# Optimization experiments

Measured on AMD Instinct MI355X. Metric: run time of the kernel, lower is better.

The kernel has to match this reference:

```python
import jax, jax.numpy as jnp
import numpy as np
import math

S, H, NH, HD = 2048, 1280, 16, 80
WIN = 64
NW = S // WIN
I = 3420
OUT = 3584
L = 8
FULL_IDX = (3, 7)
MERGE = 4  # spatial_merge_size**2
EPS = 1e-6


def setup_inputs() -> dict:
    key = jax.random.key(0)
    ks = jax.random.split(key, 16)
    w = lambda k, s: jax.random.normal(k, s, jnp.float32) * 0.02
    # rotary tables: half-dim freqs duplicated, as in Qwen2.5-VL vision rotary
    inv_freq = 1.0 / (10000.0 ** (np.arange(0, HD // 2, dtype=np.float32) / (HD // 2)))
    freqs = np.outer(np.arange(S, dtype=np.float32), inv_freq)  # [S, HD/2]
    emb = np.concatenate([freqs, freqs], axis=-1)               # [S, HD]
    return {
        "hidden_states": jax.random.normal(ks[0], (S, H), jnp.float32),
        "full_attn_masks": jnp.ones((1, 1, S, S), jnp.float32),
        "window_attn_masks": jnp.ones((NW, 1, WIN, WIN), jnp.float32),
        "cos": jnp.asarray(np.cos(emb)),
        "sin": jnp.asarray(np.sin(emb)),
        "qkv_w": w(ks[1], (L, 3 * H, H)),
        "qkv_b": w(ks[2], (L, 3 * H)),
        "proj_w": w(ks[3], (L, H, H)),
        "proj_b": w(ks[4], (L, H)),
        "norm1_w": jnp.ones((L, H), jnp.float32),
        "norm2_w": jnp.ones((L, H), jnp.float32),
        "gate_w": w(ks[5], (L, I, H)),
        "gate_b": w(ks[6], (L, I)),
        "up_w": w(ks[7], (L, I, H)),
        "up_b": w(ks[8], (L, I)),
        "down_w": w(ks[9], (L, H, I)),
        "down_b": w(ks[10], (L, H)),
        "ln_q_w": jnp.ones((H,), jnp.float32),
        "m0_w": w(ks[11], (H * MERGE, H * MERGE)),
        "m0_b": w(ks[12], (H * MERGE,)),
        "m2_w": w(ks[13], (OUT, H * MERGE)),
        "m2_b": w(ks[14], (OUT,)),
    }


def rmsnorm(x, w):
    v = jnp.mean(jnp.square(x.astype(jnp.float32)), axis=-1, keepdims=True)
    return (x * jax.lax.rsqrt(v + EPS)) * w


def rotate_half(x):
    x1, x2 = jnp.split(x, 2, axis=-1)
    return jnp.concatenate([-x2, x1], axis=-1)


def apply_rope(q, k, cos, sin):
    return q * cos + rotate_half(q) * sin, k * cos + rotate_half(k) * sin


def attn_full(x, mask, cos, sin, qkv_w, qkv_b, proj_w, proj_b):
    # x: [S, H]; mask: [1, 1, S, S] (additive)
    qkv = (x @ qkv_w.T + qkv_b).reshape(S, 3, NH, HD)
    q, k, v = [t[:, i].transpose(1, 0, 2) for i, t in [(0, qkv), (1, qkv), (2, qkv)]]  # [NH, S, HD]
    q, k = apply_rope(q, k, cos, sin)  # cos/sin [S, HD] broadcast over heads
    aw = jnp.einsum('hsd,htd->hst', q, k) / math.sqrt(HD) + mask[0]
    aw = jax.nn.softmax(aw.astype(jnp.float32), axis=-1)
    o = jnp.einsum('hst,htd->hsd', aw, v).transpose(1, 0, 2).reshape(S, NH * HD)
    return o @ proj_w.T + proj_b


def attn_window(x, mask, cos, sin, qkv_w, qkv_b, proj_w, proj_b):
    xw = x.reshape(NW, WIN, H)
    qkv = (xw @ qkv_w.T + qkv_b).reshape(NW, WIN, 3, NH, HD).transpose(2, 0, 3, 1, 4)
    q, k, v = qkv[0], qkv[1], qkv[2]
    cw = cos.reshape(NW, 1, WIN, HD)
    sw = sin.reshape(NW, 1, WIN, HD)
    q, k = apply_rope(q, k, cw, sw)
    aw = jnp.einsum('whsd,whtd->whst', q, k) / math.sqrt(HD) + mask
    aw = jax.nn.softmax(aw.astype(jnp.float32), axis=-1)
    o = jnp.einsum('whst,whtd->whsd', aw, v).transpose(0, 2, 1, 3).reshape(S, NH * HD)
    return o @ proj_w.T + proj_b


def reference(hidden_states, full_attn_masks, window_attn_masks, cos, sin,
              qkv_w, qkv_b, proj_w, proj_b, norm1_w, norm2_w,
              gate_w, gate_b, up_w, up_b, down_w, down_b,
              ln_q_w, m0_w, m0_b, m2_w, m2_b):
    NEG = jnp.finfo(jnp.float32).min
    fm = (1.0 - full_attn_masks) * NEG
    wm = (1.0 - window_attn_masks) * NEG
    x = hidden_states
    for i in range(L):
        h = rmsnorm(x, norm1_w[i])
        if i in FULL_IDX:
            a = attn_full(h, fm, cos, sin, qkv_w[i], qkv_b[i], proj_w[i], proj_b[i])
        else:
            a = attn_window(h, wm, cos, sin, qkv_w[i], qkv_b[i], proj_w[i], proj_b[i])
        x = x + a
        h = rmsnorm(x, norm2_w[i])
        mlp = (jax.nn.silu(h @ gate_w[i].T + gate_b[i]) * (h @ up_w[i].T + up_b[i])) @ down_w[i].T + down_b[i]
        x = x + mlp
    # patch merger: RMSNorm -> merge 4 tokens -> Linear-GELU-Linear
    h = rmsnorm(x, ln_q_w).reshape(-1, H * MERGE)  # [S/4, 5120]
    h = jax.nn.gelu(h @ m0_w.T + m0_b, approximate=False)
    return h @ m2_w.T + m2_b  # [S/4, OUT]
```

## Files before the change

kernel.cpp:

```cpp
#include <hip/hip_runtime.h>
#include <hip/hip_bf16.h>
#include <math.h>

#define S_LEN 2048
#define HID   1280
#define NHEADS 16
#define HDIM  80
#define HDP   96
#define VROWS 96
#define LAYERS 8
#define IDIM  3420
#define IDIMP 3456
#define MERGED 5120
#define OUTD  3584
#define LWE   19824640LL

typedef __attribute__((ext_vector_type(8))) short short8;
typedef __attribute__((ext_vector_type(4))) float f32x4;
typedef __attribute__((ext_vector_type(16))) float f32x16;
typedef unsigned int u32;
typedef __attribute__((ext_vector_type(4))) u32 u32x4;
typedef __attribute__((address_space(1))) const u32* gptr_t;
typedef __attribute__((address_space(3))) u32* lptr_t;

__device__ inline unsigned short f2b(float f){
  __hip_bfloat16 b = __float2bfloat16(f);
  return __builtin_bit_cast(unsigned short, b);
}
__device__ inline float b2f(unsigned short u){
  return __bfloat162float(__builtin_bit_cast(__hip_bfloat16, u));
}
__device__ inline unsigned pk2(float lo, float hi){
  return (unsigned)f2b(lo) | ((unsigned)f2b(hi) << 16);
}

#define NSEG 42
struct ConvSegs {
  int bpre[NSEG + 1];
  long long srcoff[NSEG];
  long long dstoff[NSEG];
  int srcbase[NSEG];
  int N[NSEG], K[NSEG], Kp[NSEG];
  int rstride[NSEG], roffs[NSEG];
};

__global__ __launch_bounds__(256) void convert_all_kernel(
    ConvSegs cs, int bstart,
    const float* __restrict__ b0, const float* __restrict__ b1,
    const float* __restrict__ b2, const float* __restrict__ b3,
    const float* __restrict__ b4, const float* __restrict__ b5,
    const float* __restrict__ b6,
    unsigned short* __restrict__ dst)
{
  const int b = blockIdx.x + bstart;
  int seg = 0;
  while (seg < NSEG - 1 && cs.bpre[seg + 1] <= b) ++seg;
  const int Kp = cs.Kp[seg], K = cs.K[seg], N = cs.N[seg];
  const int kg = Kp >> 3;
  size_t g = (size_t)(b - cs.bpre[seg]) * 256 + threadIdx.x;
  int k8 = (int)(g % kg);
  int n  = (int)(g / kg);
  int k0 = k8 * 8;
  const float* base;
  switch (cs.srcbase[seg]){
    case 0: base = b0; break; case 1: base = b1; break;
    case 2: base = b2; break; case 3: base = b3; break;
    case 4: base = b4; break; case 5: base = b5; break;
    default: base = b6; break;
  }
  const float* src = base + cs.srcoff[seg];
  u32 out0, out1, out2, out3;
  if (n < N && k0 + 8 <= K){
    const float* s = src + (size_t)n * K + k0;
    f32x4 f0 = __builtin_nontemporal_load((const f32x4*)s);
    f32x4 f1 = __builtin_nontemporal_load((const f32x4*)(s + 4));
    out0 = pk2(f0[0], f0[1]); out1 = pk2(f0[2], f0[3]);
    out2 = pk2(f1[0], f1[1]); out3 = pk2(f1[2], f1[3]);
  } else {
    u32 tmp[4];
    #pragma unroll
    for (int j = 0; j < 4; ++j){
      int ka = k0 + 2 * j;
      float lv = (n < N && ka     < K) ? src[(size_t)n * K + ka]     : 0.f;
      float hv = (n < N && ka + 1 < K) ? src[(size_t)n * K + ka + 1] : 0.f;
      tmp[j] = pk2(lv, hv);
    }
    out0 = tmp[0]; out1 = tmp[1]; out2 = tmp[2]; out3 = tmp[3];
  }
  size_t de = (size_t)cs.dstoff[seg] +
              ((size_t)n * cs.rstride[seg] + cs.roffs[seg]) * Kp + k0;
  u32x4 ov = {out0, out1, out2, out3};
  __builtin_nontemporal_store(ov, (u32x4*)(dst + de));
}

__global__ __launch_bounds__(256) void concat_bias_kernel(
    const float* __restrict__ g, const float* __restrict__ u, float* __restrict__ o)
{
  int L = blockIdx.y;
  int n = blockIdx.x * 256 + threadIdx.x;
  if (n >= 2 * IDIMP) return;
  int c = n >> 1, which = n & 1;
  float v = 0.f;
  if (c < IDIM) v = which ? u[(size_t)L * IDIM + c] : g[(size_t)L * IDIM + c];
  o[(size_t)L * 2 * IDIMP + n] = v;
}

__global__ __launch_bounds__(256) void rmsnorm_kernel(
    const float* __restrict__ x, const float* __restrict__ w,
    unsigned short* __restrict__ out, int H)
{
  int s = blockIdx.x;
  const float* row = x + (size_t)s * H;
  float ss = 0.f;
  for (int c = threadIdx.x; c < H; c += 256){ float v = row[c]; ss += v * v; }
  #pragma unroll
  for (int off = 32; off >= 1; off >>= 1) ss += __shfl_xor(ss, off, 64);
  __shared__ float red[4];
  if ((threadIdx.x & 63) == 0) red[threadIdx.x >> 6] = ss;
  __syncthreads();
  ss = red[0] + red[1] + red[2] + red[3];
  float rs = rsqrtf(ss / H + 1e-6f);
  unsigned short* orow = out + (size_t)s * H;
  for (int c = threadIdx.x; c < H; c += 256) orow[c] = f2b(row[c] * rs * w[c]);
}

template<int EPI, int BM, int BN>
__global__ __launch_bounds__(256) void gemm_kernel(
    const unsigned short* __restrict__ A, int lda,
    const unsigned short* __restrict__ B, int ldb,
    const float* __restrict__ bias, int Nact,
    void* __restrict__ Cv, int ldc,
    const float* __restrict__ res,
    int K)
{
  constexpr int MI = BM / 32;
  constexpr int NI = BN / 32;
  __shared__ __align__(16) unsigned short As[2][BM * 32];
  __shared__ __align__(16) unsigned short Bs[2][BN * 32];
  const int tid  = threadIdx.x;
  const int lane = tid & 63;
  const int wave = tid >> 6;
  const int wm = wave >> 1, wn = wave & 1;
  const int gx = gridDim.x, gy = gridDim.y;
  const int total = gx * gy;
  const int orig = blockIdx.y * gx + blockIdx.x;
  const int q8 = total >> 3, r8 = total & 7;
  const int xcd = orig & 7, loc = orig >> 3;
  const int wg = (xcd < r8 ? xcd * (q8 + 1) : r8 * (q8 + 1) + (xcd - r8) * q8) + loc;
  const int m0 = (wg % gy) * BM, n0 = (wg / gy) * BN;
  const int l16 = lane & 15, lh = lane >> 4;
  const int lrow = lane >> 2;
  const int lcol = lane & 3;
  f32x4 acc[MI][NI] = {};

  auto stage = [&](int bufi, int k0){
    #pragma unroll
    for (int j = 0; j < BM / 64; ++j){
      int chunk = wave * (BM / 64) + j;
      int row  = chunk * 16 + lrow;
      int slot = lcol ^ ((row >> 1) & 3);
      const unsigned short* srcA = A + (size_t)(m0 + row) * lda + k0 + slot * 8;
      __builtin_amdgcn_global_load_lds((gptr_t)srcA, (lptr_t)&As[bufi][chunk * 512], 16, 0, 0);
    }
    #pragma unroll
    for (int j = 0; j < BN / 64; ++j){
      int chunk = wave * (BN / 64) + j;
      int row  = chunk * 16 + lrow;
      int slot = lcol ^ ((row >> 1) & 3);
      const unsigned short* srcB = B + (size_t)(n0 + row) * ldb + k0 + slot * 8;
      __builtin_amdgcn_global_load_lds((gptr_t)srcB, (lptr_t)&Bs[bufi][chunk * 512], 16, 0, 0);
    }
  };

  const int nt = K >> 5;
  stage(0, 0);
  __syncthreads();
  int buf = 0;
  for (int t = 0; t < nt; ++t){
    if (t + 1 < nt) stage(buf ^ 1, (t + 1) << 5);
    short8 af[MI], bfr[NI];
    #pragma unroll
    for (int mi = 0; mi < MI; ++mi){
      int r = wm * (BM / 2) + mi * 16 + l16;
      int sl = lh ^ ((r >> 1) & 3);
      af[mi] = *(const short8*)&As[buf][r * 32 + sl * 8];
    }
    #pragma unroll
    for (int ni = 0; ni < NI; ++ni){
      int r = wn * (BN / 2) + ni * 16 + l16;
      int sl = lh ^ ((r >> 1) & 3);
      bfr[ni] = *(const short8*)&Bs[buf][r * 32 + sl * 8];
    }
    #pragma unroll
    for (int mi = 0; mi < MI; ++mi)
      #pragma unroll
      for (int ni = 0; ni < NI; ++ni)
        acc[mi][ni] = __builtin_amdgcn_mfma_f32_16x16x32_bf16(af[mi], bfr[ni], acc[mi][ni], 0, 0, 0);
    __syncthreads();
    buf ^= 1;
  }

  #pragma unroll
  for (int mi = 0; mi < MI; ++mi){
    int row = m0 + wm * (BM / 2) + mi * 16 + lh * 4;
    #pragma unroll
    for (int ni = 0; ni < NI; ++ni){
      int gn = n0 + wn * (BN / 2) + ni * 16 + l16;
      float bv = (gn < Nact) ? bias[gn] : 0.f;
      #pragma unroll
      for (int r2 = 0; r2 < 4; ++r2){
        float v = acc[mi][ni][r2] + bv;
        if (EPI == 4){
          float partner = __shfl_xor(v, 1);
          if (!(l16 & 1)){
            float r = v / (1.f + __expf(-v)) * partner;
            ((unsigned short*)Cv)[(size_t)(row + r2) * ldc + (gn >> 1)] = f2b(r);
          }
        } else {
          size_t offc = (size_t)(row + r2) * ldc + gn;
          if (EPI == 0)      ((float*)Cv)[offc] = v;
          else if (EPI == 1) ((float*)Cv)[offc] = res[offc] + v;
          else if (EPI == 2) ((unsigned short*)Cv)[offc] = f2b(0.5f * v * (1.0f + erff(v * 0.70710678118f)));
          else               ((unsigned short*)Cv)[offc] = f2b(v);
        }
      }
    }
  }
}

__global__ __launch_bounds__(256) void rope_split_kernel(
    const unsigned short* __restrict__ qkv, const float* __restrict__ cosT,
    const float* __restrict__ sinT,
    unsigned short* __restrict__ qo, unsigned short* __restrict__ ko,
    unsigned short* __restrict__ vt)
{
  __shared__ unsigned short vtile[80][128];
  int id = blockIdx.y * 16 + blockIdx.x;
  int logical = ((id & 7) << 5) + (id >> 3);
  const int h = logical & 15;
  const int s0 = (logical >> 4) * 128;
  const int t = threadIdx.x;
  const int sr = t >> 1, half = t & 1;
  const int s = s0 + sr;
  const unsigned short* row = qkv + (size_t)s * 3840 + h * 80;
  const float* crow = cosT + (size_t)s * 80;
  const float* srow = sinT + (size_t)s * 80;
  const float sgn = half ? 1.f : -1.f;
  #pragma unroll
  for (int g = 0; g < 5; ++g){
    int d  = half * 40 + g * 8;
    int dp = 40 - half * 40 + g * 8;
    short8 q8  = *(const short8*)(row + d);
    short8 k8  = *(const short8*)(row + 1280 + d);
    short8 qp8 = *(const short8*)(row + dp);
    short8 kp8 = *(const short8*)(row + 1280 + dp);
    short8 v8  = *(const short8*)(row + 2560 + d);
    f32x4 c0  = *(const f32x4*)(crow + d);
    f32x4 c1  = *(const f32x4*)(crow + d + 4);
    f32x4 sn0 = *(const f32x4*)(srow + d);
    f32x4 sn1 = *(const f32x4*)(srow + d + 4);
    float cc[8] = {c0[0], c0[1], c0[2], c0[3], c1[0], c1[1], c1[2], c1[3]};
    float ss[8] = {sn0[0], sn0[1], sn0[2], sn0[3], sn1[0], sn1[1], sn1[2], sn1[3]};
    short8 qo8, ko8;
    #pragma unroll
    for (int j = 0; j < 8; ++j){
      float qv = b2f((unsigned short)q8[j]);
      float kv = b2f((unsigned short)k8[j]);
      float qr = sgn * b2f((unsigned short)qp8[j]);
      float kr = sgn * b2f((unsigned short)kp8[j]);
      qo8[j] = (short)f2b(qv * cc[j] + qr * ss[j]);
      ko8[j] = (short)f2b(kv * cc[j] + kr * ss[j]);
      vtile[d + j][sr] = (unsigned short)v8[j];
    }
    size_t qkoff = ((size_t)h * S_LEN + s) * HDP + d;
    *(short8*)(qo + qkoff) = qo8;
    *(short8*)(ko + qkoff) = ko8;
  }
  {
    short8 z = {};
    size_t poff = ((size_t)h * S_LEN + s) * HDP + 80 + half * 8;
    *(short8*)(qo + poff) = z;
    *(short8*)(ko + poff) = z;
  }
  __syncthreads();
  #pragma unroll
  for (int it = 0; it < 5; ++it){
    int j = t + it * 256;
    int d = j >> 4, ch = j & 15;
    u32x4 v = *(const u32x4*)&vtile[d][ch * 8];
    *(u32x4*)(vt + ((size_t)h * VROWS + d) * S_LEN + s0 + ch * 8) = v;
  }
}

template<int PART>
__global__ __launch_bounds__(256) void flash_kernel(
    const unsigned short* __restrict__ q, const unsigned short* __restrict__ k,
    const unsigned short* __restrict__ vt, unsigned short* __restrict__ out)
{
  const int lane = threadIdx.x & 63;
  const int w = threadIdx.x >> 6;
  const int l31 = lane & 31, lh1 = lane >> 5;
  int h, qr;
  if (PART){
    int id = blockIdx.y * gridDim.x + blockIdx.x;
    int logical = ((id & 7) << 7) + (id >> 3);
    h = logical >> 6; qr = (logical & 63) * 32;
  } else {
    int id = blockIdx.y * gridDim.x + blockIdx.x;
    int logical = ((id & 7) << 5) + (id >> 3);
    h = logical >> 4; qr = (logical & 15) * 128 + w * 32;
  }
  const unsigned short* qh = q + (size_t)h * S_LEN * HDP;
  const unsigned short* kh = k + (size_t)h * S_LEN * HDP;
  const unsigned short* vh = vt + (size_t)h * VROWS * S_LEN;

  short8 qa[5];
  #pragma unroll
  for (int kc = 0; kc < 5; ++kc)
    qa[kc] = *(const short8*)(qh + (size_t)(qr + l31) * HDP + kc * 16 + lh1 * 8);

  float m_ = -1e30f, l_ = 0.f;
  f32x16 o0 = {}, o1 = {}, o2 = {};
  const int kvb = PART ? w * 512 : (qr & ~63);
  const int kve = PART ? w * 512 + 512 : (qr & ~63) + 64;
  const float scale = 0.11180339887498949f;

  for (int kvt = kvb; kvt < kve; kvt += 32){
    f32x16 sc = {};
    __builtin_amdgcn_s_setprio(1);
    #pragma unroll
    for (int kc = 0; kc < 5; ++kc){
      short8 kf = *(const short8*)(kh + (size_t)(kvt + l31) * HDP + kc * 16 + lh1 * 8);
      sc = __builtin_amdgcn_mfma_f32_32x32x16_bf16(kf, qa[kc], sc, 0, 0, 0);
    }
    __builtin_amdgcn_s_setprio(0);
    float t = sc[0];
    #pragma unroll
    for (int i = 1; i < 16; ++i) t = fmaxf(t, sc[i]);
    t = fmaxf(t, __shfl_xor(t, 32)) * scale;
    if (!__all(t <= m_ + 8.f)){
      float mnew = fmaxf(m_, t);
      float corr = __expf(m_ - mnew);
      l_ *= corr;
      #pragma unroll
      for (int i = 0; i < 16; ++i){ o0[i] *= corr; o1[i] *= corr; o2[i] *= corr; }
      m_ = mnew;
    }
    float p[16];
    float rs = 0.f;
    #pragma unroll
    for (int i = 0; i < 16; ++i){ p[i] = __expf(sc[i] * scale - m_); rs += p[i]; }
    rs += __shfl_xor(rs, 32);
    l_ += rs;
    unsigned wd0[4], wd1[4];
    #pragma unroll
    for (int j = 0; j < 2; ++j){
      unsigned Aj = pk2(p[2 * j],     p[2 * j + 1]);
      unsigned Bj = pk2(p[4 + 2 * j], p[4 + 2 * j + 1]);
      unsigned t0 = __shfl_xor(Aj, 32);
      unsigned t1 = __shfl_xor(Bj, 32);
      wd0[j]     = lh1 ? t1 : Aj;
      wd0[2 + j] = lh1 ? Bj : t0;
      Aj = pk2(p[8 + 2 * j],  p[8 + 2 * j + 1]);
      Bj = pk2(p[12 + 2 * j], p[12 + 2 * j + 1]);
      t0 = __shfl_xor(Aj, 32);
      t1 = __shfl_xor(Bj, 32);
      wd1[j]     = lh1 ? t1 : Aj;
      wd1[2 + j] = lh1 ? Bj : t0;
    }
    __builtin_amdgcn_s_setprio(1);
    #pragma unroll
    for (int kc2 = 0; kc2 < 2; ++kc2){
      u32x4 uw = kc2 ? u32x4{wd1[0], wd1[1], wd1[2], wd1[3]}
                     : u32x4{wd0[0], wd0[1], wd0[2], wd0[3]};
      short8 pb = __builtin_bit_cast(short8, uw);
      const unsigned short* vb = vh + kvt + kc2 * 16 + lh1 * 8;
      o0 = __builtin_amdgcn_mfma_f32_32x32x16_bf16(
          *(const short8*)(vb + (size_t)(l31)      * S_LEN), pb, o0, 0, 0, 0);
      o1 = __builtin_amdgcn_mfma_f32_32x32x16_bf16(
          *(const short8*)(vb + (size_t)(32 + l31) * S_LEN), pb, o1, 0, 0, 0);
      o2 = __builtin_amdgcn_mfma_f32_32x32x16_bf16(
          *(const short8*)(vb + (size_t)(64 + l31) * S_LEN), pb, o2, 0, 0, 0);
    }
    __builtin_amdgcn_s_setprio(0);
  }

  if (PART){
    __shared__ float of[80][33];
    __shared__ float mlsh[4][32][2];
    __shared__ float Lsh[32];
    __shared__ unsigned short ot2[32][88];
    if (lane < 32){ mlsh[w][l31][0] = m_; mlsh[w][l31][1] = l_; }
    __syncthreads();
    float M = fmaxf(fmaxf(mlsh[0][l31][0], mlsh[1][l31][0]),
                    fmaxf(mlsh[2][l31][0], mlsh[3][l31][0]));
    float L = 0.f;
    #pragma unroll
    for (int c = 0; c < 4; ++c) L += __expf(mlsh[c][l31][0] - M) * mlsh[c][l31][1];
    float wgt = __expf(m_ - M);
    if (w == 0 && lane < 32) Lsh[l31] = L;
    #pragma unroll
    for (int rnd = 0; rnd < 4; ++rnd){
      if (w == rnd){
        #pragma unroll
        for (int i = 0; i < 16; ++i){
          int dl = (i & 3) + 8 * (i >> 2) + 4 * lh1;
          if (rnd == 0){
            of[dl][l31]      = wgt * o0[i];
            of[32 + dl][l31] = wgt * o1[i];
            if (dl < 16) of[64 + dl][l31] = wgt * o2[i];
          } else {
            of[dl][l31]      += wgt * o0[i];
            of[32 + dl][l31] += wgt * o1[i];
            if (dl < 16) of[64 + dl][l31] += wgt * o2[i];
          }
        }
      }
      __syncthreads();
    }
    const int tq = threadIdx.x & 31, ds0 = (threadIdx.x >> 5) * 10;
    float Lq = Lsh[tq];
    #pragma unroll
    for (int j = 0; j < 10; ++j)
      ot2[tq][ds0 + j] = f2b(of[ds0 + j][tq] / Lq);
    __syncthreads();
    if (threadIdx.x < 64){
      int qq = threadIdx.x >> 1, half = threadIdx.x & 1;
      #pragma unroll
      for (int j2 = 0; j2 < 20; ++j2){
        unsigned v = *(const unsigned*)&ot2[qq][half * 40 + j2 * 2];
        *(unsigned*)&out[(size_t)(qr + qq) * HID + h * HDIM + half * 40 + j2 * 2] = v;
      }
    }
  } else {
    __shared__ unsigned short ot[4][32][88];
    float inv = 1.f / l_;
    #pragma unroll
    for (int r = 0; r < 16; ++r){
      int dl = (r & 3) + 8 * (r >> 2) + 4 * lh1;
      ot[w][l31][dl]      = f2b(o0[r] * inv);
      ot[w][l31][32 + dl] = f2b(o1[r] * inv);
      if (dl < 16) ot[w][l31][64 + dl] = f2b(o2[r] * inv);
    }
    int qq = lane >> 1, half = lane & 1;
    #pragma unroll
    for (int j = 0; j < 20; ++j){
      unsigned v = *(const unsigned*)&ot[w][qq][half * 40 + j * 2];
      *(unsigned*)&out[(size_t)(qr + qq) * HID + h * HDIM + half * 40 + j * 2] = v;
    }
  }
}

extern "C" void kernel_launch(void* const* d_in, const int* in_sizes, int n_in,
                              void* d_out, int out_size, void* d_ws, size_t ws_size,
                              hipStream_t stream)
{
  const float* hidden = (const float*)d_in[0];
  const float* cosT   = (const float*)d_in[3];
  const float* sinT   = (const float*)d_in[4];
  const float* qkv_w  = (const float*)d_in[5];
  const float* qkv_b  = (const float*)d_in[6];
  const float* proj_w = (const float*)d_in[7];
  const float* proj_b = (const float*)d_in[8];
  const float* norm1_w= (const float*)d_in[9];
  const float* norm2_w= (const float*)d_in[10];
  const float* gate_w = (const float*)d_in[11];
  const float* gate_b = (const float*)d_in[12];
  const float* up_w   = (const float*)d_in[13];
  const float* up_b   = (const float*)d_in[14];
  const float* down_w = (const float*)d_in[15];
  const float* down_b = (const float*)d_in[16];
  const float* ln_q_w = (const float*)d_in[17];
  const float* m0_w   = (const float*)d_in[18];
  const float* m0_b   = (const float*)d_in[19];
  const float* m2_w   = (const float*)d_in[20];
  const float* m2_b   = (const float*)d_in[21];

  char* ws = (char*)d_ws;
  size_t off = 0;
  auto carve = [&](size_t bytes)->char*{
    char* p = ws + off; off += (bytes + 255) & ~(size_t)255; return p;
  };
  float*          x    = (float*)         carve((size_t)S_LEN * HID * 4);
  unsigned short* hbuf = (unsigned short*)carve((size_t)S_LEN * HID * 2);
  unsigned short* qkvb = (unsigned short*)carve((size_t)S_LEN * 3840 * 2);
  unsigned short* qp   = (unsigned short*)carve((size_t)NHEADS * S_LEN * HDP * 2);
  unsigned short* kp   = (unsigned short*)carve((size_t)NHEADS * S_LEN * HDP * 2);
  unsigned short* vtb  = (unsigned short*)carve((size_t)NHEADS * VROWS * S_LEN * 2);
  unsigned short* ao   = (unsigned short*)carve((size_t)S_LEN * HID * 2);
  unsigned short* mlp  = (unsigned short*)carve((size_t)S_LEN * IDIMP * 2);
  unsigned short* mg   = (unsigned short*)carve((size_t)512 * MERGED * 2);
  float*          cbias= (float*)         carve((size_t)LAYERS * 2 * IDIMP * 4);
  unsigned short* wbf  = (unsigned short*)carve((size_t)203161600 * 2);
  (void)ws_size; (void)in_sizes; (void)n_in; (void)out_size;

  ConvSegs cs;
  int totalblocks = 0;
  {
    int si = 0;
    auto add = [&](int base, long long soff, long long doff, int N, int K,
                   int Np, int Kp, int rstride, int roffs){
      cs.bpre[si] = totalblocks;
      cs.srcbase[si] = base; cs.srcoff[si] = soff; cs.dstoff[si] = doff;
      cs.N[si] = N; cs.K[si] = K; cs.Kp[si] = Kp;
      cs.rstride[si] = rstride; cs.roffs[si] = roffs;
      long long groups = (long long)Np * (Kp >> 3);
      totalblocks += (int)((groups + 255) / 256);
      ++si;
    };
    for (long long i = 0; i < LAYERS; ++i){
      add(0, i * 3840LL * HID,        i * LWE + 0,        3840, HID, 3840, HID, 1, 0);
      add(1, i * (long long)HID * HID, i * LWE + 4915200,  HID, HID, HID, HID, 1, 0);
      add(2, i * (long long)IDIM * HID, i * LWE + 6553600,  IDIM, HID, IDIMP, HID, 2, 0);
      add(3, i * (long long)IDIM * HID, i * LWE + 6553600,  IDIM, HID, IDIMP, HID, 2, 1);
      add(4, i * (long long)HID * IDIM, i * LWE + 15400960, HID, IDIM, HID, IDIMP, 1, 0);
    }
    add(5, 0, 8 * LWE,            MERGED, MERGED, MERGED, MERGED, 1, 0);
    add(6, 0, 8 * LWE + 26214400, OUTD,   MERGED, OUTD,   MERGED, 1, 0);
    cs.bpre[NSEG] = totalblocks;
  }

  {
    int chunk = (totalblocks + 3) / 4;
    for (int c = 0; c < 4; ++c){
      int bs = c * chunk;
      int nb = (bs + chunk <= totalblocks) ? chunk : (totalblocks - bs);
      if (nb > 0)
        convert_all_kernel<<<nb, 256, 0, stream>>>(
            cs, bs, qkv_w, proj_w, gate_w, up_w, down_w, m0_w, m2_w, wbf);
    }
  }
  concat_bias_kernel<<<dim3(27, LAYERS), 256, 0, stream>>>(gate_b, up_b, cbias);
  hipMemcpyAsync(x, hidden, (size_t)S_LEN * HID * 4, hipMemcpyDeviceToDevice, stream);

  for (int i = 0; i < LAYERS; ++i){
    unsigned short* wl = wbf + (size_t)i * LWE;
    unsigned short* wqkv = wl;
    unsigned short* wproj= wl + 4915200;
    unsigned short* wgu  = wl + 6553600;
    unsigned short* wdown= wl + 15400960;

    rmsnorm_kernel<<<S_LEN, 256, 0, stream>>>(x, norm1_w + (size_t)i * HID, hbuf, HID);
    gemm_kernel<3,128,128><<<dim3(30, 16), 256, 0, stream>>>(
        hbuf, HID, wqkv, HID, qkv_b + (size_t)i * 3840, 3840,
        qkvb, 3840, nullptr, HID);
    rope_split_kernel<<<dim3(NHEADS, 16), 256, 0, stream>>>(qkvb, cosT, sinT, qp, kp, vtb);
    if (i == 3 || i == 7){
      flash_kernel<1><<<dim3(64, 16), 256, 0, stream>>>(qp, kp, vtb, ao);
    } else {
      flash_kernel<0><<<dim3(16, 16), 256, 0, stream>>>(qp, kp, vtb, ao);
    }
    gemm_kernel<1,64,64><<<dim3(20, 32), 256, 0, stream>>>(
        ao, HID, wproj, HID, proj_b + (size_t)i * HID, HID,
        x, HID, x, HID);
    rmsnorm_kernel<<<S_LEN, 256, 0, stream>>>(x, norm2_w + (size_t)i * HID, hbuf, HID);
    gemm_kernel<4,128,128><<<dim3(54, 16), 256, 0, stream>>>(
        hbuf, HID, wgu, HID, cbias + (size_t)i * 2 * IDIMP, 2 * IDIMP,
        mlp, IDIMP, nullptr, HID);
    gemm_kernel<1,64,64><<<dim3(20, 32), 256, 0, stream>>>(
        mlp, IDIMP, wdown, IDIMP, down_b + (size_t)i * HID, HID,
        x, HID, x, IDIMP);
  }
  unsigned short* wm0 = wbf + 8 * LWE;
  unsigned short* wm2 = wm0 + (size_t)MERGED * MERGED;
  rmsnorm_kernel<<<S_LEN, 256, 0, stream>>>(x, ln_q_w, hbuf, HID);
  gemm_kernel<2,64,64><<<dim3(80, 8), 256, 0, stream>>>(
      hbuf, MERGED, wm0, MERGED, m0_b, MERGED, mg, MERGED, nullptr, MERGED);
  gemm_kernel<0,64,64><<<dim3(56, 8), 256, 0, stream>>>(
      mg, MERGED, wm2, MERGED, m2_b, OUTD, d_out, OUTD, nullptr, MERGED);
}
```

Baseline: 2.465 ms.

## Fuse RoPE and split into window attention kernel via shared memory

For the window-attention layers, a new kernel applies rotary embedding to q/k and transposes v straight into shared memory, then runs the 64-token window attention from LDS. This removes the separate rope_split launch and the global-memory round trip of padded q, k and transposed v for those layers. Full-attention layers keep the old path, now as a dedicated non-templated kernel. In exchange the fused kernel uses a large shared-memory footprint, which may lower occupancy.

```diff
diff --git a/kernel.cpp b/kernel.cpp
--- a/kernel.cpp
+++ b/kernel.cpp
@@ -292,54 +292,103 @@
   }
 }
 
-template<int PART>
-__global__ __launch_bounds__(256) void flash_kernel(
-    const unsigned short* __restrict__ q, const unsigned short* __restrict__ k,
-    const unsigned short* __restrict__ vt, unsigned short* __restrict__ out)
+#define QKPAD 104
+#define VPAD  136
+__global__ __launch_bounds__(256) void rope_window_kernel(
+    const unsigned short* __restrict__ qkv, const float* __restrict__ cosT,
+    const float* __restrict__ sinT, unsigned short* __restrict__ out)
 {
-  const int lane = threadIdx.x & 63;
-  const int w = threadIdx.x >> 6;
+  __shared__ __align__(16) unsigned short qs[128][QKPAD];
+  __shared__ __align__(16) unsigned short ks[128][QKPAD];
+  __shared__ __align__(16) unsigned short vtile[96][VPAD];
+  __shared__ unsigned short ot[4][32][88];
+  int id = blockIdx.y * 16 + blockIdx.x;
+  int logical = ((id & 7) << 5) + (id >> 3);
+  const int h = logical & 15;
+  const int s0 = (logical >> 4) * 128;
+  const int t = threadIdx.x;
+  {
+    const int sr = t >> 1, half = t & 1;
+    const int s = s0 + sr;
+    const unsigned short* row = qkv + (size_t)s * 3840 + h * 80;
+    const float* crow = cosT + (size_t)s * 80;
+    const float* srow = sinT + (size_t)s * 80;
+    const float sgn = half ? 1.f : -1.f;
+    #pragma unroll
+    for (int g = 0; g < 5; ++g){
+      int d  = half * 40 + g * 8;
+      int dp = 40 - half * 40 + g * 8;
+      short8 q8  = *(const short8*)(row + d);
+      short8 k8  = *(const short8*)(row + 1280 + d);
+      short8 qp8 = *(const short8*)(row + dp);
+      short8 kp8 = *(const short8*)(row + 1280 + dp);
+      short8 v8  = *(const short8*)(row + 2560 + d);
+      f32x4 c0  = *(const f32x4*)(crow + d);
+      f32x4 c1  = *(const f32x4*)(crow + d + 4);
+      f32x4 sn0 = *(const f32x4*)(srow + d);
+      f32x4 sn1 = *(const f32x4*)(srow + d + 4);
+      float cc[8] = {c0[0], c0[1], c0[2], c0[3], c1[0], c1[1], c1[2], c1[3]};
+      float ss[8] = {sn0[0], sn0[1], sn0[2], sn0[3], sn1[0], sn1[1], sn1[2], sn1[3]};
+      short8 qo8, ko8;
+      #pragma unroll
+      for (int j = 0; j < 8; ++j){
+        float qv = b2f((unsigned short)q8[j]);
+        float kv = b2f((unsigned short)k8[j]);
+        float qr = sgn * b2f((unsigned short)qp8[j]);
+        float kr = sgn * b2f((unsigned short)kp8[j]);
+        qo8[j] = (short)f2b(qv * cc[j] + qr * ss[j]);
+        ko8[j] = (short)f2b(kv * cc[j] + kr * ss[j]);
+        vtile[d + j][sr] = (unsigned short)v8[j];
+      }
+      *(short8*)&qs[sr][d] = qo8;
+      *(short8*)&ks[sr][d] = ko8;
+    }
+    short8 z = {};
+    *(short8*)&qs[sr][80 + half * 8] = z;
+    *(short8*)&ks[sr][80 + half * 8] = z;
+    #pragma unroll
+    for (int r9 = 0; r9 < 2; ++r9){
+      int task = t + r9 * 256;
+      if (task < 16 * 17){
+        int rr = task / 17, cc2 = (task % 17) * 8;
+        *(short8*)&vtile[80 + rr][cc2] = z;
+      }
+    }
+  }
+  __syncthreads();
+
+  const int lane = t & 63;
+  const int w = t >> 6;
   const int l31 = lane & 31, lh1 = lane >> 5;
-  int h, qr;
-  if (PART){
-    int id = blockIdx.y * gridDim.x + blockIdx.x;
-    int logical = ((id & 7) << 7) + (id >> 3);
-    h = logical >> 6; qr = (logical & 63) * 32;
-  } else {
-    int id = blockIdx.y * gridDim.x + blockIdx.x;
-    int logical = ((id & 7) << 5) + (id >> 3);
-    h = logical >> 4; qr = (logical & 15) * 128 + w * 32;
-  }
-  const unsigned short* qh = q + (size_t)h * S_LEN * HDP;
-  const unsigned short* kh = k + (size_t)h * S_LEN * HDP;
-  const unsigned short* vh = vt + (size_t)h * VROWS * S_LEN;
+  const int qrl = w * 32;
+  const int kv0 = (w >> 1) * 64;
 
   short8 qa[5];
   #pragma unroll
   for (int kc = 0; kc < 5; ++kc)
-    qa[kc] = *(const short8*)(qh + (size_t)(qr + l31) * HDP + kc * 16 + lh1 * 8);
+    qa[kc] = *(const short8*)&qs[qrl + l31][kc * 16 + lh1 * 8];
 
   float m_ = -1e30f, l_ = 0.f;
   f32x16 o0 = {}, o1 = {}, o2 = {};
-  const int kvb = PART ? w * 512 : (qr & ~63);
-  const int kve = PART ? w * 512 + 512 : (qr & ~63) + 64;
   const float scale = 0.11180339887498949f;
 
-  for (int kvt = kvb; kvt < kve; kvt += 32){
+  #pragma unroll
+  for (int step = 0; step < 2; ++step){
+    int kvl = kv0 + step * 32;
     f32x16 sc = {};
     __builtin_amdgcn_s_setprio(1);
     #pragma unroll
     for (int kc = 0; kc < 5; ++kc){
-      short8 kf = *(const short8*)(kh + (size_t)(kvt + l31) * HDP + kc * 16 + lh1 * 8);
+      short8 kf = *(const short8*)&ks[kvl + l31][kc * 16 + lh1 * 8];
       sc = __builtin_amdgcn_mfma_f32_32x32x16_bf16(kf, qa[kc], sc, 0, 0, 0);
     }
     __builtin_amdgcn_s_setprio(0);
-    float t = sc[0];
-    #pragma unroll
-    for (int i = 1; i < 16; ++i) t = fmaxf(t, sc[i]);
-    t = fmaxf(t, __shfl_xor(t, 32)) * scale;
-    if (!__all(t <= m_ + 8.f)){
-      float mnew = fmaxf(m_, t);
+    float tmax = sc[0];
+    #pragma unroll
+    for (int i = 1; i < 16; ++i) tmax = fmaxf(tmax, sc[i]);
+    tmax = fmaxf(tmax, __shfl_xor(tmax, 32)) * scale;
+    if (!__all(tmax <= m_ + 8.f)){
+      float mnew = fmaxf(m_, tmax);
       float corr = __expf(m_ - mnew);
       l_ *= corr;
       #pragma unroll
@@ -374,6 +423,106 @@
       u32x4 uw = kc2 ? u32x4{wd1[0], wd1[1], wd1[2], wd1[3]}
                      : u32x4{wd0[0], wd0[1], wd0[2], wd0[3]};
       short8 pb = __builtin_bit_cast(short8, uw);
+      int sv = kvl + kc2 * 16 + lh1 * 8;
+      o0 = __builtin_amdgcn_mfma_f32_32x32x16_bf16(
+          *(const short8*)&vtile[l31][sv],      pb, o0, 0, 0, 0);
+      o1 = __builtin_amdgcn_mfma_f32_32x32x16_bf16(
+          *(const short8*)&vtile[32 + l31][sv], pb, o1, 0, 0, 0);
+      o2 = __builtin_amdgcn_mfma_f32_32x32x16_bf16(
+          *(const short8*)&vtile[64 + l31][sv], pb, o2, 0, 0, 0);
+    }
+    __builtin_amdgcn_s_setprio(0);
+  }
+
+  float inv = 1.f / l_;
+  #pragma unroll
+  for (int r = 0; r < 16; ++r){
+    int dl = (r & 3) + 8 * (r >> 2) + 4 * lh1;
+    ot[w][l31][dl]      = f2b(o0[r] * inv);
+    ot[w][l31][32 + dl] = f2b(o1[r] * inv);
+    if (dl < 16) ot[w][l31][64 + dl] = f2b(o2[r] * inv);
+  }
+  int qq = lane >> 1, half2 = lane & 1;
+  #pragma unroll
+  for (int j = 0; j < 20; ++j){
+    unsigned v = *(const unsigned*)&ot[w][qq][half2 * 40 + j * 2];
+    *(unsigned*)&out[(size_t)(s0 + qrl + qq) * HID + h * HDIM + half2 * 40 + j * 2] = v;
+  }
+}
+
+__global__ __launch_bounds__(256) void flash_full_kernel(
+    const unsigned short* __restrict__ q, const unsigned short* __restrict__ k,
+    const unsigned short* __restrict__ vt, unsigned short* __restrict__ out)
+{
+  const int lane = threadIdx.x & 63;
+  const int w = threadIdx.x >> 6;
+  const int l31 = lane & 31, lh1 = lane >> 5;
+  int id = blockIdx.y * gridDim.x + blockIdx.x;
+  int logical = ((id & 7) << 7) + (id >> 3);
+  const int h = logical >> 6;
+  const int qr = (logical & 63) * 32;
+  const unsigned short* qh = q + (size_t)h * S_LEN * HDP;
+  const unsigned short* kh = k + (size_t)h * S_LEN * HDP;
+  const unsigned short* vh = vt + (size_t)h * VROWS * S_LEN;
+
+  short8 qa[5];
+  #pragma unroll
+  for (int kc = 0; kc < 5; ++kc)
+    qa[kc] = *(const short8*)(qh + (size_t)(qr + l31) * HDP + kc * 16 + lh1 * 8);
+
+  float m_ = -1e30f, l_ = 0.f;
+  f32x16 o0 = {}, o1 = {}, o2 = {};
+  const float scale = 0.11180339887498949f;
+
+  for (int kvt = w * 512; kvt < w * 512 + 512; kvt += 32){
+    f32x16 sc = {};
+    __builtin_amdgcn_s_setprio(1);
+    #pragma unroll
+    for (int kc = 0; kc < 5; ++kc){
+      short8 kf = *(const short8*)(kh + (size_t)(kvt + l31) * HDP + kc * 16 + lh1 * 8);
+      sc = __builtin_amdgcn_mfma_f32_32x32x16_bf16(kf, qa[kc], sc, 0, 0, 0);
+    }
+    __builtin_amdgcn_s_setprio(0);
+    float t = sc[0];
+    #pragma unroll
+    for (int i = 1; i < 16; ++i) t = fmaxf(t, sc[i]);
+    t = fmaxf(t, __shfl_xor(t, 32)) * scale;
+    if (!__all(t <= m_ + 8.f)){
+      float mnew = fmaxf(m_, t);
+      float corr = __expf(m_ - mnew);
+      l_ *= corr;
+      #pragma unroll
+      for (int i = 0; i < 16; ++i){ o0[i] *= corr; o1[i] *= corr; o2[i] *= corr; }
+      m_ = mnew;
+    }
+    float p[16];
+    float rs = 0.f;
+    #pragma unroll
+    for (int i = 0; i < 16; ++i){ p[i] = __expf(sc[i] * scale - m_); rs += p[i]; }
+    rs += __shfl_xor(rs, 32);
+    l_ += rs;
+    unsigned wd0[4], wd1[4];
+    #pragma unroll
+    for (int j = 0; j < 2; ++j){
+      unsigned Aj = pk2(p[2 * j],     p[2 * j + 1]);
+      unsigned Bj = pk2(p[4 + 2 * j], p[4 + 2 * j + 1]);
+      unsigned t0 = __shfl_xor(Aj, 32);
+      unsigned t1 = __shfl_xor(Bj, 32);
+      wd0[j]     = lh1 ? t1 : Aj;
+      wd0[2 + j] = lh1 ? Bj : t0;
+      Aj = pk2(p[8 + 2 * j],  p[8 + 2 * j + 1]);
+      Bj = pk2(p[12 + 2 * j], p[12 + 2 * j + 1]);
+      t0 = __shfl_xor(Aj, 32);
+      t1 = __shfl_xor(Bj, 32);
+      wd1[j]     = lh1 ? t1 : Aj;
+      wd1[2 + j] = lh1 ? Bj : t0;
+    }
+    __builtin_amdgcn_s_setprio(1);
+    #pragma unroll
+    for (int kc2 = 0; kc2 < 2; ++kc2){
+      u32x4 uw = kc2 ? u32x4{wd1[0], wd1[1], wd1[2], wd1[3]}
+                     : u32x4{wd0[0], wd0[1], wd0[2], wd0[3]};
+      short8 pb = __builtin_bit_cast(short8, uw);
       const unsigned short* vb = vh + kvt + kc2 * 16 + lh1 * 8;
       o0 = __builtin_amdgcn_mfma_f32_32x32x16_bf16(
           *(const short8*)(vb + (size_t)(l31)      * S_LEN), pb, o0, 0, 0, 0);
@@ -385,68 +534,50 @@
     __builtin_amdgcn_s_setprio(0);
   }
 
-  if (PART){
-    __shared__ float of[80][33];
-    __shared__ float mlsh[4][32][2];
-    __shared__ float Lsh[32];
-    __shared__ unsigned short ot2[32][88];
-    if (lane < 32){ mlsh[w][l31][0] = m_; mlsh[w][l31][1] = l_; }
-    __syncthreads();
-    float M = fmaxf(fmaxf(mlsh[0][l31][0], mlsh[1][l31][0]),
-                    fmaxf(mlsh[2][l31][0], mlsh[3][l31][0]));
-    float L = 0.f;
-    #pragma unroll
-    for (int c = 0; c < 4; ++c) L += __expf(mlsh[c][l31][0] - M) * mlsh[c][l31][1];
-    float wgt = __expf(m_ - M);
-    if (w == 0 && lane < 32) Lsh[l31] = L;
-    #pragma unroll
-    for (int rnd = 0; rnd < 4; ++rnd){
-      if (w == rnd){
-        #pragma unroll
-        for (int i = 0; i < 16; ++i){
-          int dl = (i & 3) + 8 * (i >> 2) + 4 * lh1;
-          if (rnd == 0){
-            of[dl][l31]      = wgt * o0[i];
-            of[32 + dl][l31] = wgt * o1[i];
-            if (dl < 16) of[64 + dl][l31] = wgt * o2[i];
-          } else {
-            of[dl][l31]      += wgt * o0[i];
-            of[32 + dl][l31] += wgt * o1[i];
-            if (dl < 16) of[64 + dl][l31] += wgt * o2[i];
-          }
+  __shared__ float of[80][33];
+  __shared__ float mlsh[4][32][2];
+  __shared__ float Lsh[32];
+  __shared__ unsigned short ot2[32][88];
+  if (lane < 32){ mlsh[w][l31][0] = m_; mlsh[w][l31][1] = l_; }
+  __syncthreads();
+  float M = fmaxf(fmaxf(mlsh[0][l31][0], mlsh[1][l31][0]),
+                  fmaxf(mlsh[2][l31][0], mlsh[3][l31][0]));
+  float L = 0.f;
+  #pragma unroll
+  for (int c = 0; c < 4; ++c) L += __expf(mlsh[c][l31][0] - M) * mlsh[c][l31][1];
+  float wgt = __expf(m_ - M);
+  if (w == 0 && lane < 32) Lsh[l31] = L;
+  #pragma unroll
+  for (int rnd = 0; rnd < 4; ++rnd){
+    if (w == rnd){
+      #pragma unroll
+      for (int i = 0; i < 16; ++i){
+        int dl = (i & 3) + 8 * (i >> 2) + 4 * lh1;
+        if (rnd == 0){
+          of[dl][l31]      = wgt * o0[i];
+          of[32 + dl][l31] = wgt * o1[i];
+          if (dl < 16) of[64 + dl][l31] = wgt * o2[i];
+        } else {
+          of[dl][l31]      += wgt * o0[i];
+          of[32 + dl][l31] += wgt * o1[i];
+          if (dl < 16) of[64 + dl][l31] += wgt * o2[i];
         }
       }
-      __syncthreads();
-    }
-    const int tq = threadIdx.x & 31, ds0 = (threadIdx.x >> 5) * 10;
-    float Lq = Lsh[tq];
-    #pragma unroll
-    for (int j = 0; j < 10; ++j)
-      ot2[tq][ds0 + j] = f2b(of[ds0 + j][tq] / Lq);
+    }
     __syncthreads();
-    if (threadIdx.x < 64){
-      int qq = threadIdx.x >> 1, half = threadIdx.x & 1;
-      #pragma unroll
-      for (int j2 = 0; j2 < 20; ++j2){
-        unsigned v = *(const unsigned*)&ot2[qq][half * 40 + j2 * 2];
-        *(unsigned*)&out[(size_t)(qr + qq) * HID + h * HDIM + half * 40 + j2 * 2] = v;
-      }
-    }
-  } else {
-    __shared__ unsigned short ot[4][32][88];
-    float inv = 1.f / l_;
-    #pragma unroll
-    for (int r = 0; r < 16; ++r){
-      int dl = (r & 3) + 8 * (r >> 2) + 4 * lh1;
-      ot[w][l31][dl]      = f2b(o0[r] * inv);
-      ot[w][l31][32 + dl] = f2b(o1[r] * inv);
-      if (dl < 16) ot[w][l31][64 + dl] = f2b(o2[r] * inv);
-    }
-    int qq = lane >> 1, half = lane & 1;
-    #pragma unroll
-    for (int j = 0; j < 20; ++j){
-      unsigned v = *(const unsigned*)&ot[w][qq][half * 40 + j * 2];
-      *(unsigned*)&out[(size_t)(qr + qq) * HID + h * HDIM + half * 40 + j * 2] = v;
+  }
+  const int tq = threadIdx.x & 31, ds0 = (threadIdx.x >> 5) * 10;
+  float Lq = Lsh[tq];
+  #pragma unroll
+  for (int j = 0; j < 10; ++j)
+    ot2[tq][ds0 + j] = f2b(of[ds0 + j][tq] / Lq);
+  __syncthreads();
+  if (threadIdx.x < 64){
+    int qq = threadIdx.x >> 1, half = threadIdx.x & 1;
+    #pragma unroll
+    for (int j2 = 0; j2 < 20; ++j2){
+      unsigned v = *(const unsigned*)&ot2[qq][half * 40 + j2 * 2];
+      *(unsigned*)&out[(size_t)(qr + qq) * HID + h * HDIM + half * 40 + j2 * 2] = v;
     }
   }
 }
@@ -544,11 +675,11 @@
     gemm_kernel<3,128,128><<<dim3(30, 16), 256, 0, stream>>>(
         hbuf, HID, wqkv, HID, qkv_b + (size_t)i * 3840, 3840,
         qkvb, 3840, nullptr, HID);
-    rope_split_kernel<<<dim3(NHEADS, 16), 256, 0, stream>>>(qkvb, cosT, sinT, qp, kp, vtb);
     if (i == 3 || i == 7){
-      flash_kernel<1><<<dim3(64, 16), 256, 0, stream>>>(qp, kp, vtb, ao);
+      rope_split_kernel<<<dim3(NHEADS, 16), 256, 0, stream>>>(qkvb, cosT, sinT, qp, kp, vtb);
+      flash_full_kernel<<<dim3(64, 16), 256, 0, stream>>>(qp, kp, vtb, ao);
     } else {
-      flash_kernel<0><<<dim3(16, 16), 256, 0, stream>>>(qp, kp, vtb, ao);
+      rope_window_kernel<<<dim3(16, 16), 256, 0, stream>>>(qkvb, cosT, sinT, ao);
     }
     gemm_kernel<1,64,64><<<dim3(20, 32), 256, 0, stream>>>(
         ao, HID, wproj, HID, proj_b + (size_t)i * HID, HID,
```

Result: faster. 2.406 ms (-2.4%).
